# Optimization experiments

Hardware: AMD Instinct MI355X
Metric: run time of the kernel (lower is better)

The kernel has to match this reference:

```python
import jax, jax.numpy as jnp
import numpy as np

B, C, H, W = 32, 256, 56, 56
KS, NK = 7, 16
EPS = 1e-5

def setup_inputs() -> dict:
    key = jax.random.key(0)
    ks = jax.random.split(key, 9)
    return {
        "x": jax.random.normal(ks[0], (B, C, H, W), jnp.float32),
        "bn_gamma": jax.random.normal(ks[1], (C,), jnp.float32) * 0.1 + 1.0,
        "bn_beta": jax.random.normal(ks[2], (C,), jnp.float32) * 0.1,
        "bn_mean": jax.random.normal(ks[3], (C,), jnp.float32) * 0.1,
        "bn_var": jax.random.uniform(ks[4], (C,), jnp.float32) + 0.5,
        "q_w": jax.random.normal(ks[5], (C, C), jnp.float32) / np.sqrt(C),
        "k_w": jax.random.normal(ks[6], (NK, C), jnp.float32) / np.sqrt(C),
        "kernel_bank": jax.random.normal(ks[7], (NK, KS * KS), jnp.float32),
        "bias": jnp.zeros((C,), jnp.float32),
    }

def reference(x, bn_gamma, bn_beta, bn_mean, bn_var, q_w, k_w, kernel_bank, bias):
    b, c, h, w = x.shape
    temp = 2.0 * c  # self.temp = channels * 2
    # BatchNorm2d (eval mode: affine with running stats)
    scale = bn_gamma / jnp.sqrt(bn_var + EPS)
    xn = (x - bn_mean[:, None, None]) * scale[:, None, None] + bn_beta[:, None, None]
    xf = xn.reshape(b, c, h * w)                       # [B, C, HW]
    Q = jnp.einsum('oc,bcn->bon', q_w, xf)             # 1x1 conv -> [B, C, HW]
    K = jnp.einsum('kc,bcn->bnk', k_w, xf)             # 1x1 conv -> [B, HW, NK]
    attn = jax.nn.softmax(jnp.einsum('bcn,bnk->bck', Q, K) / temp, axis=2)  # [B, C, NK]
    wgt = jnp.einsum('bck,ke->bce', attn, kernel_bank)  # [B, C, KS*KS]
    wgt = wgt.reshape(b * c, 1, KS, KS)                # per-sample per-channel kernels
    pad = KS // 2
    # dynamic depthwise conv: groups = B*C  (torch padding='same')
    out = jax.lax.conv_general_dilated(
        x.reshape(1, b * c, h, w), wgt,
        window_strides=(1, 1), padding=[(pad, pad), (pad, pad)],
        feature_group_count=b * c,
        dimension_numbers=('NCHW', 'OIHW', 'NCHW'))
    return out.reshape(b, c, h, w) + bias[None, :, None, None]
```

## Files before the change

### kernel.cpp

```cpp
#include <hip/hip_runtime.h>
#include <hip/hip_bf16.h>

#define BATCH 32
#define CH    256
#define HWPX  3136
#define WIDTH 56
#define NK    16
#define NSLAB 28
#define NSUB  4
#define WGTS  52
#define EPSV  1e-5f

__device__ __forceinline__ unsigned pk_bf2(float a, float b) {
    __hip_bfloat16 ha = __float2bfloat16(a), hb = __float2bfloat16(b);
    unsigned short ua = *reinterpret_cast<unsigned short*>(&ha);
    unsigned short ub = *reinterpret_cast<unsigned short*>(&hb);
    return ((unsigned)ub << 16) | ua;
}
__device__ __forceinline__ float up_lo(unsigned v) { return __uint_as_float(v << 16); }
__device__ __forceinline__ float up_hi(unsigned v) { return __uint_as_float(v & 0xffff0000u); }

__global__ __launch_bounds__(64) void kkvec(
    const float* __restrict__ x,
    const float* __restrict__ gamma, const float* __restrict__ beta,
    const float* __restrict__ mean,  const float* __restrict__ var,
    const float* __restrict__ kw,    unsigned short* __restrict__ Kpart)
{
    const int sub = blockIdx.x / 784;
    const int pb  = blockIdx.x % 784;
    const int job = pb * 64 + threadIdx.x;
    const int b   = job / 1568;
    const int px2 = job % 1568;
    const int cbase = sub * 64;
    const float* xp = x + ((size_t)b * CH + cbase) * HWPX + px2 * 2;

    float acc0[NK], acc1[NK];
#pragma unroll
    for (int k = 0; k < NK; ++k) { acc0[k] = 0.f; acc1[k] = 0.f; }

    for (int c0 = 0; c0 < 64; c0 += 8) {
        float2 v[8];
#pragma unroll
        for (int i = 0; i < 8; ++i)
            v[i] = *(const float2*)(xp + (size_t)(c0 + i) * HWPX);
#pragma unroll
        for (int i = 0; i < 8; ++i) {
            const int c = cbase + c0 + i;
            const float sc = gamma[c] * rsqrtf(var[c] + EPSV);
            const float sh = fmaf(-mean[c], sc, beta[c]);
            v[i].x = fmaf(v[i].x, sc, sh);
            v[i].y = fmaf(v[i].y, sc, sh);
        }
#pragma unroll
        for (int k = 0; k < NK; ++k) {
            const float4 w0 = *(const float4*)(kw + k * CH + cbase + c0);
            const float4 w1 = *(const float4*)(kw + k * CH + cbase + c0 + 4);
            acc0[k] = fmaf(v[0].x, w0.x, acc0[k]); acc1[k] = fmaf(v[0].y, w0.x, acc1[k]);
            acc0[k] = fmaf(v[1].x, w0.y, acc0[k]); acc1[k] = fmaf(v[1].y, w0.y, acc1[k]);
            acc0[k] = fmaf(v[2].x, w0.z, acc0[k]); acc1[k] = fmaf(v[2].y, w0.z, acc1[k]);
            acc0[k] = fmaf(v[3].x, w0.w, acc0[k]); acc1[k] = fmaf(v[3].y, w0.w, acc1[k]);
            acc0[k] = fmaf(v[4].x, w1.x, acc0[k]); acc1[k] = fmaf(v[4].y, w1.x, acc1[k]);
            acc0[k] = fmaf(v[5].x, w1.y, acc0[k]); acc1[k] = fmaf(v[5].y, w1.y, acc1[k]);
            acc0[k] = fmaf(v[6].x, w1.z, acc0[k]); acc1[k] = fmaf(v[6].y, w1.z, acc1[k]);
            acc0[k] = fmaf(v[7].x, w1.w, acc0[k]); acc1[k] = fmaf(v[7].y, w1.w, acc1[k]);
        }
    }

    unsigned short* op = Kpart + ((size_t)sub * BATCH * HWPX + (size_t)b * HWPX + px2 * 2) * NK;
    uint4* op4 = (uint4*)op;
    op4[0] = make_uint4(pk_bf2(acc0[0],  acc0[1]),  pk_bf2(acc0[2],  acc0[3]),
                        pk_bf2(acc0[4],  acc0[5]),  pk_bf2(acc0[6],  acc0[7]));
    op4[1] = make_uint4(pk_bf2(acc0[8],  acc0[9]),  pk_bf2(acc0[10], acc0[11]),
                        pk_bf2(acc0[12], acc0[13]), pk_bf2(acc0[14], acc0[15]));
    op4[2] = make_uint4(pk_bf2(acc1[0],  acc1[1]),  pk_bf2(acc1[2],  acc1[3]),
                        pk_bf2(acc1[4],  acc1[5]),  pk_bf2(acc1[6],  acc1[7]));
    op4[3] = make_uint4(pk_bf2(acc1[8],  acc1[9]),  pk_bf2(acc1[10], acc1[11]),
                        pk_bf2(acc1[12], acc1[13]), pk_bf2(acc1[14], acc1[15]));
}

__global__ __launch_bounds__(256) void ksum(
    const unsigned short* __restrict__ Kpart, float* __restrict__ Kbuf)
{
    const int i = blockIdx.x * 256 + threadIdx.x;
    const uint2* p = (const uint2*)Kpart;
    float4 s = make_float4(0.f, 0.f, 0.f, 0.f);
#pragma unroll
    for (int s2 = 0; s2 < NSUB; ++s2) {
        const uint2 v = p[(size_t)s2 * 401408 + i];
        s.x += up_lo(v.x); s.y += up_hi(v.x);
        s.z += up_lo(v.y); s.w += up_hi(v.y);
    }
    ((float4*)Kbuf)[i] = s;
}

__global__ __launch_bounds__(256) void kpmat(
    const float* __restrict__ x,
    const float* __restrict__ gamma, const float* __restrict__ beta,
    const float* __restrict__ mean,  const float* __restrict__ var,
    const float* __restrict__ Kbuf,  float* __restrict__ Pp)
{
    const int b  = blockIdx.x / NSLAB;
    const int nb = blockIdx.x % NSLAB;
    const int n0 = nb * 112;
    const int c  = threadIdx.x;

    const float sc = gamma[c] * rsqrtf(var[c] + EPSV);
    const float sh = fmaf(-mean[c], sc, beta[c]);

    const float4* xr = (const float4*)(x + ((size_t)b * CH + c) * HWPX + n0);
    const float*  Kp = Kbuf + ((size_t)b * HWPX + n0) * NK;

    float acc[NK];
#pragma unroll
    for (int k = 0; k < NK; ++k) acc[k] = 0.f;

#pragma unroll 4
    for (int j = 0; j < 28; ++j) {
        const float4 xv = xr[j];
        float v[4];
        v[0] = fmaf(xv.x, sc, sh); v[1] = fmaf(xv.y, sc, sh);
        v[2] = fmaf(xv.z, sc, sh); v[3] = fmaf(xv.w, sc, sh);
#pragma unroll
        for (int d = 0; d < 4; ++d) {
            const float vd = v[d];
#pragma unroll
            for (int kq = 0; kq < 4; ++kq) {
                const float4 kv = *(const float4*)(Kp + ((j*4 + d) * NK) + kq*4);
                acc[kq*4+0] = fmaf(vd, kv.x, acc[kq*4+0]);
                acc[kq*4+1] = fmaf(vd, kv.y, acc[kq*4+1]);
                acc[kq*4+2] = fmaf(vd, kv.z, acc[kq*4+2]);
                acc[kq*4+3] = fmaf(vd, kv.w, acc[kq*4+3]);
            }
        }
    }
    float4* op = (float4*)(Pp + (((size_t)b * NSLAB + nb) * CH + c) * NK);
#pragma unroll
    for (int kq = 0; kq < 4; ++kq)
        op[kq] = make_float4(acc[kq*4+0], acc[kq*4+1], acc[kq*4+2], acc[kq*4+3]);
}

__global__ __launch_bounds__(256) void kpred(
    const float* __restrict__ Pp, float* __restrict__ P)
{
    const int idx = blockIdx.x * 256 + threadIdx.x;
    const int b = idx >> 12;
    const int e = idx & 4095;
    const float* p = Pp + (size_t)b * NSLAB * 4096 + e;
    float s = 0.f;
#pragma unroll
    for (int nb = 0; nb < NSLAB; ++nb) s += p[(size_t)nb * 4096];
    P[idx] = s;
}

__global__ __launch_bounds__(256) void ksoft(
    const float* __restrict__ P, const float* __restrict__ qw,
    const float* __restrict__ bank, float* __restrict__ wgt)
{
    const int b  = blockIdx.x >> 3;
    const int cb = blockIdx.x & 7;
    const int tid = threadIdx.x;

    __shared__ float s_P[CH * NK];
    __shared__ float s_red[32 * 8 * NK];
    __shared__ float s_S[32 * NK];
    __shared__ float s_attn[32 * NK];

    for (int idx = tid; idx < CH * NK; idx += 256)
        s_P[idx] = P[(size_t)b * CH * NK + idx];
    __syncthreads();

    const int c_l = tid & 31, sub = tid >> 5;
    const int c = cb * 32 + c_l;
    float a[NK];
#pragma unroll
    for (int k = 0; k < NK; ++k) a[k] = 0.f;
    const float* qrow = qw + (size_t)c * CH + sub * 32;
    for (int j = 0; j < 32; ++j) {
        const float qv = qrow[j];
        const float4* p4 = (const float4*)&s_P[(sub * 32 + j) * NK];
#pragma unroll
        for (int kq = 0; kq < 4; ++kq) {
            const float4 pv = p4[kq];
            a[kq*4+0] = fmaf(qv, pv.x, a[kq*4+0]);
            a[kq*4+1] = fmaf(qv, pv.y, a[kq*4+1]);
            a[kq*4+2] = fmaf(qv, pv.z, a[kq*4+2]);
            a[kq*4+3] = fmaf(qv, pv.w, a[kq*4+3]);
        }
    }
#pragma unroll
    for (int kq = 0; kq < 4; ++kq)
        *(float4*)&s_red[(c_l * 8 + sub) * NK + kq*4] =
            make_float4(a[kq*4+0], a[kq*4+1], a[kq*4+2], a[kq*4+3]);
    __syncthreads();

    for (int idx = tid; idx < 32 * NK; idx += 256) {
        const int cl = idx >> 4, k = idx & 15;
        float s = 0.f;
#pragma unroll
        for (int s2 = 0; s2 < 8; ++s2) s += s_red[(cl * 8 + s2) * NK + k];
        s_S[idx] = s * (1.f / 512.f);
    }
    __syncthreads();

    if (tid < 32) {
        float l[NK];
#pragma unroll
        for (int k = 0; k < NK; ++k) l[k] = s_S[tid * NK + k];
        float m = l[0];
#pragma unroll
        for (int k = 1; k < NK; ++k) m = fmaxf(m, l[k]);
        float sum = 0.f;
#pragma unroll
        for (int k = 0; k < NK; ++k) { l[k] = __expf(l[k] - m); sum += l[k]; }
        const float inv = 1.f / sum;
#pragma unroll
        for (int k = 0; k < NK; ++k) s_attn[tid * NK + k] = l[k] * inv;
    }
    __syncthreads();

    for (int idx = tid; idx < 32 * 49; idx += 256) {
        const int cl = idx / 49, e = idx - cl * 49;
        float wv = 0.f;
#pragma unroll
        for (int k = 0; k < NK; ++k)
            wv = fmaf(s_attn[cl * NK + k], bank[k * 49 + e], wv);
        wgt[((size_t)b * CH + cb * 32 + cl) * WGTS + e] = wv;
    }
}

__global__ __launch_bounds__(256) void kconv(
    const float* __restrict__ x, const float* __restrict__ wgt,
    const float* __restrict__ bias, float* __restrict__ out)
{
    const int t  = threadIdx.x;
    const int pl = t >> 4;
    const int q  = t & 15;
    const int qc = q < 14 ? q : 13;
    const int h  = blockIdx.x & 1;
    const int plane = (blockIdx.x >> 1) * 16 + pl;
    const int ho = h * 28;
    const bool qlo = (q == 0), qhi = (q >= 13);
    const float bv = bias[plane & 255];

    float4 wv[13];
    const float4* wp4 = (const float4*)(wgt + (size_t)plane * WGTS);
#pragma unroll
    for (int i = 0; i < 13; ++i) wv[i] = wp4[i];
#define WTAP(idx) ((idx)%4==0 ? wv[(idx)/4].x : (idx)%4==1 ? wv[(idx)/4].y : \
                   (idx)%4==2 ? wv[(idx)/4].z : wv[(idx)/4].w)

    const float* xrow = x   + (size_t)plane * HWPX + 4 * qc;
    float*       orow = out + (size_t)plane * HWPX + 4 * qc;

    float a[7][4];
#pragma unroll
    for (int i = 0; i < 7; ++i)
#pragma unroll
        for (int ix = 0; ix < 4; ++ix) a[i][ix] = bv;

    const float4 z4 = make_float4(0.f, 0.f, 0.f, 0.f);
    int ir0 = ho - 3;
    float4 vc = (0 <= ir0 && ir0 < 56) ? *(const float4*)(xrow + ir0 * WIDTH) : z4;

#pragma unroll 7
    for (int j = 0; j < 35; ++j) {
        const int snew = j % 7;
#pragma unroll
        for (int ix = 0; ix < 4; ++ix) a[snew][ix] = bv;

        const int irn = ho - 3 + j + 1;
        float4 vn = (0 <= irn && irn < 56 && j + 1 < 35)
                        ? *(const float4*)(xrow + irn * WIDTH) : z4;

        float rr1 = __shfl_up(vc.y, 1), rr2 = __shfl_up(vc.z, 1), rr3 = __shfl_up(vc.w, 1);
        float rr8 = __shfl_down(vc.x, 1), rr9 = __shfl_down(vc.y, 1), rr10 = __shfl_down(vc.z, 1);
        float rr[11];
        rr[1] = qlo ? 0.f : rr1;  rr[2] = qlo ? 0.f : rr2;  rr[3] = qlo ? 0.f : rr3;
        rr[4] = vc.x; rr[5] = vc.y; rr[6] = vc.z; rr[7] = vc.w;
        rr[8] = qhi ? 0.f : rr8;  rr[9] = qhi ? 0.f : rr9;  rr[10] = qhi ? 0.f : rr10;

#pragma unroll
        for (int i = 0; i < 7; ++i) {
            const int ky = 6 - i;
            const int s  = (j + i + 1) % 7;
#pragma unroll
            for (int kx = 0; kx < 7; ++kx) {
                const float wk = WTAP(ky * 7 + kx);
#pragma unroll
                for (int ix = 0; ix < 4; ++ix)
                    a[s][ix] = fmaf(wk, rr[ix + kx + 1], a[s][ix]);
            }
        }

        if (j >= 6 && j < 34) {
            const int o  = ho + j - 6;
            const int sd = (j + 1) % 7;
            if (q < 14)
                *(float4*)(orow + o * WIDTH) =
                    make_float4(a[sd][0], a[sd][1], a[sd][2], a[sd][3]);
        }
        vc = vn;
    }
#undef WTAP
}

extern "C" void kernel_launch(void* const* d_in, const int* in_sizes, int n_in,
                              void* d_out, int out_size, void* d_ws, size_t ws_size,
                              hipStream_t stream)
{
    const float* x     = (const float*)d_in[0];
    const float* gamma = (const float*)d_in[1];
    const float* beta  = (const float*)d_in[2];
    const float* mean  = (const float*)d_in[3];
    const float* var   = (const float*)d_in[4];
    const float* qw    = (const float*)d_in[5];
    const float* kw    = (const float*)d_in[6];
    const float* bank  = (const float*)d_in[7];
    const float* bias  = (const float*)d_in[8];
    float* out = (float*)d_out;

    const size_t KBUF_F = (size_t)BATCH * HWPX * NK;
    const size_t PP_F   = (size_t)BATCH * NSLAB * CH * NK;

    float* ws    = (float*)d_ws;
    float* Kbuf  = ws;
    unsigned short* Kpart = (unsigned short*)(ws + KBUF_F);
    float* Pp    = ws + KBUF_F;
    float* P     = ws + KBUF_F + PP_F;
    float* wgt   = P + (size_t)BATCH * CH * NK;

    kkvec<<<dim3(NSUB * 784),   dim3(64),  0, stream>>>(x, gamma, beta, mean, var, kw, Kpart);
    ksum <<<dim3(1568),         dim3(256), 0, stream>>>(Kpart, Kbuf);
    kpmat<<<dim3(BATCH * NSLAB),dim3(256), 0, stream>>>(x, gamma, beta, mean, var, Kbuf, Pp);
    kpred<<<dim3(512),          dim3(256), 0, stream>>>(Pp, P);
    ksoft<<<dim3(BATCH * 8),    dim3(256), 0, stream>>>(P, qw, bank, wgt);
    kconv<<<dim3(BATCH * CH / 8), dim3(256), 0, stream>>>(x, wgt, bias, out);
}
```

Measured before the change: 131.3 us.

## Retile depthwise conv to one plane per block with 4x4 register tiles

The depthwise 7x7 conv kernel moves from a sliding-window scheme (each thread streams 28 output rows with a 7-slot rolling accumulator) to one block per plane, with each thread computing a 4x4 output tile. The aim is more parallelism and shorter serial dependency chains per thread. In exchange, each thread rereads 10 input rows for 4 outputs, doubling input row loads, and about a quarter of the threads in each block sit idle (16x16 grid for a 14x14 tile layout).

```diff
diff --git a/kernel.cpp b/kernel.cpp
--- a/kernel.cpp
+++ b/kernel.cpp
@@ -232,13 +232,12 @@
     const float* __restrict__ x, const float* __restrict__ wgt,
     const float* __restrict__ bias, float* __restrict__ out)
 {
-    const int t  = threadIdx.x;
-    const int pl = t >> 4;
-    const int q  = t & 15;
-    const int qc = q < 14 ? q : 13;
-    const int h  = blockIdx.x & 1;
-    const int plane = (blockIdx.x >> 1) * 16 + pl;
-    const int ho = h * 28;
+    const int t   = threadIdx.x;
+    const int q   = t & 15;
+    const int tyv = t >> 4;
+    const int qc  = q  < 14 ? q  : 13;
+    const int tyc = tyv < 14 ? tyv : 13;
+    const int plane = blockIdx.x;
     const bool qlo = (q == 0), qhi = (q >= 13);
     const float bv = bias[plane & 255];
 
@@ -252,25 +251,21 @@
     const float* xrow = x   + (size_t)plane * HWPX + 4 * qc;
     float*       orow = out + (size_t)plane * HWPX + 4 * qc;
 
-    float a[7][4];
-#pragma unroll
-    for (int i = 0; i < 7; ++i)
-#pragma unroll
-        for (int ix = 0; ix < 4; ++ix) a[i][ix] = bv;
-
+    float acc[4][4];
+#pragma unroll
+    for (int iy = 0; iy < 4; ++iy)
+#pragma unroll
+        for (int ix = 0; ix < 4; ++ix) acc[iy][ix] = bv;
+
+    const int r0 = tyc * 4 - 3;
     const float4 z4 = make_float4(0.f, 0.f, 0.f, 0.f);
-    int ir0 = ho - 3;
-    float4 vc = (0 <= ir0 && ir0 < 56) ? *(const float4*)(xrow + ir0 * WIDTH) : z4;
-
-#pragma unroll 7
-    for (int j = 0; j < 35; ++j) {
-        const int snew = j % 7;
-#pragma unroll
-        for (int ix = 0; ix < 4; ++ix) a[snew][ix] = bv;
-
-        const int irn = ho - 3 + j + 1;
-        float4 vn = (0 <= irn && irn < 56 && j + 1 < 35)
-                        ? *(const float4*)(xrow + irn * WIDTH) : z4;
+    float4 vc = (r0 >= 0) ? *(const float4*)(xrow + r0 * WIDTH) : z4;
+
+#pragma unroll
+    for (int ir = 0; ir < 10; ++ir) {
+        const int rn = r0 + ir + 1;
+        float4 vn = (ir < 9 && rn >= 0 && rn < 56)
+                        ? *(const float4*)(xrow + rn * WIDTH) : z4;
 
         float rr1 = __shfl_up(vc.y, 1), rr2 = __shfl_up(vc.z, 1), rr3 = __shfl_up(vc.w, 1);
         float rr8 = __shfl_down(vc.x, 1), rr9 = __shfl_down(vc.y, 1), rr10 = __shfl_down(vc.z, 1);
@@ -280,26 +275,27 @@
         rr[8] = qhi ? 0.f : rr8;  rr[9] = qhi ? 0.f : rr9;  rr[10] = qhi ? 0.f : rr10;
 
 #pragma unroll
-        for (int i = 0; i < 7; ++i) {
-            const int ky = 6 - i;
-            const int s  = (j + i + 1) % 7;
+        for (int iy = 0; iy < 4; ++iy) {
+            const int ky = ir - iy;
+            if (ky < 0 || ky > 6) continue;
 #pragma unroll
             for (int kx = 0; kx < 7; ++kx) {
                 const float wk = WTAP(ky * 7 + kx);
 #pragma unroll
                 for (int ix = 0; ix < 4; ++ix)
-                    a[s][ix] = fmaf(wk, rr[ix + kx + 1], a[s][ix]);
+                    acc[iy][ix] = fmaf(wk, rr[ix + kx + 1], acc[iy][ix]);
             }
         }
-
-        if (j >= 6 && j < 34) {
-            const int o  = ho + j - 6;
-            const int sd = (j + 1) % 7;
-            if (q < 14)
-                *(float4*)(orow + o * WIDTH) =
-                    make_float4(a[sd][0], a[sd][1], a[sd][2], a[sd][3]);
-        }
         vc = vn;
+    }
+
+    if (q < 14 && tyv < 14) {
+#pragma unroll
+        for (int iy = 0; iy < 4; ++iy) {
+            const int o = tyc * 4 + iy;
+            *(float4*)(orow + o * WIDTH) =
+                make_float4(acc[iy][0], acc[iy][1], acc[iy][2], acc[iy][3]);
+        }
     }
 #undef WTAP
 }
@@ -334,5 +330,5 @@
     kpmat<<<dim3(BATCH * NSLAB),dim3(256), 0, stream>>>(x, gamma, beta, mean, var, Kbuf, Pp);
     kpred<<<dim3(512),          dim3(256), 0, stream>>>(Pp, P);
     ksoft<<<dim3(BATCH * 8),    dim3(256), 0, stream>>>(P, qw, bank, wgt);
-    kconv<<<dim3(BATCH * CH / 8), dim3(256), 0, stream>>>(x, wgt, bias, out);
-}
+    kconv<<<dim3(BATCH * CH),   dim3(256), 0, stream>>>(x, wgt, bias, out);
+}
```

Result: faster. 124.1 us (-5.5%).
